# Kernel optimization log

Hardware: AMD Instinct MI355X
Metric: run time of the kernel (lower is better)

The kernel has to match this reference:

```python
import jax, jax.numpy as jnp
import numpy as np

SIG_G = [1.0, 1.0, 1.0]
LAYER_DIMS = [256, 128, 64]
N_ITER = 20
ALPHA = 0.01
B = 4096


def _cayley(g):
    # Cayley table C[a,b,c]: e_a * e_b = C[a,b,a^b] * e_{a^b} for diagonal metric g.
    n = len(g)
    nb = 1 << n
    C = np.zeros((nb, nb, nb), np.float32)
    for a in range(nb):
        for b in range(nb):
            # canonical reordering sign
            s = 0
            aa = a >> 1
            while aa:
                s += bin(aa & b).count('1')
                aa >>= 1
            sign = -1.0 if (s & 1) else 1.0
            # metric contribution from repeated generators
            for i in range(n):
                if (a >> i) & 1 and (b >> i) & 1:
                    sign *= g[i]
            C[a, b, a ^ b] = sign
    return jnp.asarray(C)


def _reverse_signs(n):
    # reverse: blade of grade k gets sign (-1)^(k*(k-1)/2)
    nb = 1 << n
    k = np.array([bin(i).count('1') for i in range(nb)])
    return jnp.asarray(((-1.0) ** (k * (k - 1) // 2)).astype(np.float32))


CAYLEY = _cayley(SIG_G)   # [8, 8, 8], sparse (one nonzero per (a,b))
REV = _reverse_signs(len(SIG_G))  # [8]


def _gp(x, W):
    # geometric product 'linear layer': x [B, Din, nb], W [Dout, Din, nb] -> [B, Dout, nb]
    return jnp.einsum('nja,ijb,abc->nic', x, W, CAYLEY, optimize=True)


def setup_inputs() -> dict:
    key = jax.random.key(0)
    ks = jax.random.split(key, 5)
    nb = 1 << len(SIG_G)
    x = jax.random.normal(ks[0], (B, LAYER_DIMS[0], nb), jnp.float32)
    W1 = jax.random.normal(ks[1], (LAYER_DIMS[0], LAYER_DIMS[1], nb), jnp.float32) * 0.01
    W2 = jax.random.normal(ks[2], (LAYER_DIMS[1], LAYER_DIMS[2], nb), jnp.float32) * 0.01
    h1 = jax.random.normal(ks[3], (B, LAYER_DIMS[1], nb), jnp.float32) * 0.001
    h2 = jax.random.normal(ks[4], (B, LAYER_DIMS[2], nb), jnp.float32) * 0.001
    return {'x': x, 'W1': W1, 'W2': W2, 'h1': h1, 'h2': h2}


def reference(x, W1, W2, h1, h2):
    states = [x, h1, h2]
    weights = [W1, W2]
    L = len(states)
    for _ in range(N_ITER):
        for l in range(1, L):
            W = weights[l - 1]                      # [D_{l-1}, D_l, nb]
            pred_prev = _gp(states[l], W)           # [B, D_{l-1}, nb]
            err_prev = states[l - 1] - pred_prev
            W_rev_T = jnp.transpose(W * REV, (1, 0, 2))  # reverse + transpose(0,1)
            grad = -_gp(err_prev, W_rev_T)          # [B, D_l, nb]
            if l < L - 1:
                pred_curr = _gp(states[l + 1], weights[l])
                grad = grad + (states[l] - pred_curr)
            grad = jnp.clip(grad, -1.0, 1.0)
            states[l] = states[l] - ALPHA * grad
    return tuple(states)
```

## Files before the change

kernel.cpp:

```cpp
#include <hip/hip_runtime.h>

#define N_ITER 20
#define ALPHA 0.01f

typedef unsigned short ushort_t;
typedef __attribute__((ext_vector_type(8))) short bf16x8;
typedef __attribute__((ext_vector_type(16))) float f32x16;

__device__ __forceinline__ float csign(int a, int b) {
    int s = 0;
    for (int aa = a >> 1; aa; aa >>= 1) s += __popc(aa & b);
    return (s & 1) ? -1.0f : 1.0f;
}

__device__ __forceinline__ float revsign(int b) {
    int k = __popc(b);
    return ((k * (k - 1) / 2) & 1) ? -1.0f : 1.0f;
}

__device__ __forceinline__ ushort_t f2bf(float f) {
    union { float f; unsigned u; } v;
    v.f = f;
    unsigned r = v.u + 0x7fffu + ((v.u >> 16) & 1u);
    return (ushort_t)(r >> 16);
}

__device__ __forceinline__ size_t swz64(int r, int k, int K) {
    return (size_t)r * K + (k & ~63) + ((((k >> 3) ^ r) & 7) << 3) + (k & 7);
}

__device__ __forceinline__ void async16(const void* g, void* l) {
    __builtin_amdgcn_global_load_lds((const __attribute__((address_space(1))) void*)g,
                                     (__attribute__((address_space(3))) void*)l, 16, 0, 0);
}

__global__ void build_M_kernel(const float* __restrict__ W, ushort_t* __restrict__ MfA,
                               ushort_t* __restrict__ Mrbt, ushort_t* __restrict__ Mrneg,
                               ushort_t* __restrict__ Mbtneg, int P, int Q) {
    int idx = blockIdx.x * blockDim.x + threadIdx.x;
    int total = P * Q * 64;
    if (idx >= total) return;
    int c = idx & 7;
    int a = (idx >> 3) & 7;
    int pq = idx >> 6;
    int q = pq % Q;
    int p = pq / Q;
    int b = a ^ c;
    float w = W[((size_t)p * Q + q) * 8 + b];
    float fw = csign(a, b) * w;
    float rw = csign(a, b) * revsign(b) * w;
    MfA[swz64(q * 8 + a, p * 8 + c, P * 8)] = f2bf(fw);
    Mrbt[swz64(q * 8 + c, p * 8 + a, P * 8)] = f2bf(rw);
    if (Mrneg) Mrneg[swz64(q * 8 + c, p * 8 + a, P * 8)] = f2bf(-rw);
    if (Mbtneg) Mbtneg[swz64(p * 8 + c, q * 8 + a, Q * 8)] = f2bf(-fw);
}

__global__ void f2bf_swz_kernel(const float* __restrict__ in, ushort_t* __restrict__ out,
                                int n, int kshift) {
    int i = blockIdx.x * blockDim.x + threadIdx.x;
    if (i >= n) return;
    int K = 1 << kshift;
    int r = i >> kshift;
    int k = i & (K - 1);
    out[swz64(r, k, K)] = f2bf(in[i]);
}

template <int MODE, int BM, int BN, bool ADDI>
__device__ __forceinline__ void gemm_body(ushort_t* __restrict__ S,
                                          const ushort_t* __restrict__ A,
                                          const ushort_t* __restrict__ BT, int K,
                                          const ushort_t* __restrict__ A2,
                                          const ushort_t* __restrict__ BT2, int K2,
                                          const float* __restrict__ Xf,
                                          const float* __restrict__ Rf,
                                          float* __restrict__ Hout,
                                          ushort_t* __restrict__ Bout,
                                          float* __restrict__ Fout,
                                          int N, int bx, int by) {
    constexpr int FI = BM / 64;
    constexpr int FJ = BN / 64;
    constexpr int CPW = (BM + BN) / 32;
    constexpr int SZ = (BM + BN) * 64;

    const int t = threadIdx.x;
    const int lane = t & 63;
    const int w = t >> 6;
    const int wr = w >> 1;
    const int wc = w & 1;
    const int l31 = lane & 31;
    const int lh = lane >> 5;
    const int row0 = by * BM;
    const int col0 = bx * BN;
    const int srow = lane >> 3;
    const int sk = (lane & 7) * 8;
    const int sw7 = l31 & 7;

    f32x16 acc[FI][FJ];
#pragma unroll
    for (int i = 0; i < FI; ++i)
#pragma unroll
        for (int j = 0; j < FJ; ++j)
#pragma unroll
            for (int r = 0; r < 16; ++r) acc[i][j][r] = 0.0f;

    const ushort_t* gpA[CPW];
    const ushort_t* gpB[CPW];
    int lofs[CPW];
#pragma unroll
    for (int cc = 0; cc < CPW; ++cc) {
        int ch = cc * 4 + w;
        int r8 = ch * 8;
        lofs[cc] = ch * 512;
        if (r8 < BM) {
            gpA[cc] = A + (size_t)(row0 + r8 + srow) * K + sk;
            gpB[cc] = A2 ? (A2 + (size_t)(row0 + r8 + srow) * K2 + sk) : nullptr;
        } else {
            gpA[cc] = BT + (size_t)(col0 + r8 - BM + srow) * K + sk;
            gpB[cc] = BT2 ? (BT2 + (size_t)(col0 + r8 - BM + srow) * K2 + sk) : nullptr;
        }
    }

    const int T1 = K >> 6;
    const int T2 = K2 >> 6;
    const int Ttot = T1 + T2;

    auto stage = [&](int tt, ushort_t* Sb) {
        if (tt < T1) {
#pragma unroll
            for (int cc = 0; cc < CPW; ++cc)
                async16(gpA[cc] + (size_t)tt * 64, &Sb[lofs[cc]]);
        } else {
            const int tl = tt - T1;
#pragma unroll
            for (int cc = 0; cc < CPW; ++cc)
                async16(gpB[cc] + (size_t)tl * 64, &Sb[lofs[cc]]);
        }
    };

    stage(0, S);
    __syncthreads();

    ushort_t* Sc = S;
    ushort_t* Sn = S + SZ;
    for (int tt = 0; tt < Ttot; ++tt) {
        if (tt + 1 < Ttot) stage(tt + 1, Sn);

        bf16x8 af[4][FI], bfm[4][FJ];
#pragma unroll
        for (int s = 0; s < 4; ++s) {
            int pos = ((2 * s + lh) ^ sw7) * 8;
#pragma unroll
            for (int i = 0; i < FI; ++i)
                af[s][i] = *(const bf16x8*)&Sc[(wr * (BM / 2) + i * 32 + l31) * 64 + pos];
#pragma unroll
            for (int j = 0; j < FJ; ++j)
                bfm[s][j] = *(const bf16x8*)&Sc[(BM + wc * (BN / 2) + j * 32 + l31) * 64 + pos];
        }
#pragma unroll
        for (int s = 0; s < 4; ++s)
#pragma unroll
            for (int i = 0; i < FI; ++i)
#pragma unroll
                for (int j = 0; j < FJ; ++j)
                    acc[i][j] = __builtin_amdgcn_mfma_f32_32x32x16_bf16(af[s][i], bfm[s][j],
                                                                        acc[i][j], 0, 0, 0);
        __syncthreads();
        ushort_t* tmp = Sc; Sc = Sn; Sn = tmp;
    }

#pragma unroll
    for (int i = 0; i < FI; ++i) {
#pragma unroll
        for (int j = 0; j < FJ; ++j) {
#pragma unroll
            for (int r = 0; r < 16; ++r) {
                int row = row0 + wr * (BM / 2) + i * 32 + (r & 3) + 8 * (r >> 2) + 4 * lh;
                int col = col0 + wc * (BN / 2) + j * 32 + l31;
                size_t off = (size_t)row * N + col;
                float v = acc[i][j][r];
                if (MODE == 1) {
                    Fout[off] = v;
                } else if (MODE == 2) {
                    float h = Xf[off];
                    float g = fminf(fmaxf(v - Rf[off], -1.0f), 1.0f);
                    float hn = h - ALPHA * g;
                    Hout[off] = hn;
                    Bout[swz64(row, col, N)] = f2bf(hn);
                } else if (MODE == 3) {
                    float h = Xf[off];
                    float g = fminf(fmaxf(v, -1.0f), 1.0f);
                    float hn = h - ALPHA * g;
                    Hout[off] = hn;
                    Bout[swz64(row, col, N)] = f2bf(hn);
                } else {
                    float vv = v + ((ADDI && row == col) ? 1.0f : 0.0f);
                    Bout[swz64(col, row, N)] = f2bf(vv);
                }
            }
        }
    }
}

template <int MODE, int BM, int BN, bool ADDI>
__global__ __launch_bounds__(256) void gemm_k(const ushort_t* __restrict__ A,
                                              const ushort_t* __restrict__ BT, int K,
                                              const ushort_t* __restrict__ A2,
                                              const ushort_t* __restrict__ BT2, int K2,
                                              const float* __restrict__ Xf,
                                              const float* __restrict__ Rf,
                                              float* __restrict__ Hout,
                                              ushort_t* __restrict__ Bout,
                                              float* __restrict__ Fout, int N) {
    __shared__ ushort_t S[2 * (BM + BN) * 64];
    gemm_body<MODE, BM, BN, ADDI>(S, A, BT, K, A2, BT2, K2, Xf, Rf, Hout, Bout, Fout, N,
                                  blockIdx.x, blockIdx.y);
}

extern "C" void kernel_launch(void* const* d_in, const int* in_sizes, int n_in,
                              void* d_out, int out_size, void* d_ws, size_t ws_size,
                              hipStream_t stream) {
    const float* X  = (const float*)d_in[0];
    const float* W1 = (const float*)d_in[1];
    const float* W2 = (const float*)d_in[2];
    const float* h1 = (const float*)d_in[3];
    const float* h2 = (const float*)d_in[4];
    float* out = (float*)d_out;

    const size_t szX  = (size_t)4096 * 2048;
    const size_t szH1 = (size_t)4096 * 1024;
    const size_t szH2 = (size_t)4096 * 512;

    float* outX = out;
    float* H1 = out + szX;
    float* H2 = H1 + szH1;

    ushort_t* M1fwdA  = (ushort_t*)d_ws;
    ushort_t* M1rbt   = M1fwdA + (size_t)1024 * 2048;
    ushort_t* M2fwdA  = M1rbt + (size_t)1024 * 2048;
    ushort_t* M2rbt   = M2fwdA + (size_t)512 * 1024;
    ushort_t* M2rneg  = M2rbt + (size_t)512 * 1024;
    ushort_t* M2btneg = M2rneg + (size_t)512 * 1024;
    ushort_t* GmT1p   = M2btneg + (size_t)1024 * 512;
    ushort_t* GmT2    = GmT1p + (size_t)1024 * 1024;
    ushort_t* Xb      = GmT2 + (size_t)512 * 512;
    ushort_t* H1bA    = Xb + szX;
    ushort_t* H1bB    = H1bA + szH1;
    ushort_t* H2bA    = H1bB + szH1;
    ushort_t* H2bB    = H2bA + szH2;
    float*    R       = (float*)(H2bB + szH2);

    build_M_kernel<<<(256 * 128 * 64 + 255) / 256, 256, 0, stream>>>(
        W1, M1fwdA, M1rbt, nullptr, nullptr, 256, 128);
    build_M_kernel<<<(128 * 64 * 64 + 255) / 256, 256, 0, stream>>>(
        W2, M2fwdA, M2rbt, M2rneg, M2btneg, 128, 64);

    hipMemcpyAsync(H1, h1, szH1 * sizeof(float), hipMemcpyDeviceToDevice, stream);
    hipMemcpyAsync(H2, h2, szH2 * sizeof(float), hipMemcpyDeviceToDevice, stream);
    f2bf_swz_kernel<<<(int)((szX + 255) / 256), 256, 0, stream>>>(X, Xb, (int)szX, 11);
    f2bf_swz_kernel<<<(int)((szH1 + 255) / 256), 256, 0, stream>>>(h1, H1bA, (int)szH1, 10);
    f2bf_swz_kernel<<<(int)((szH2 + 255) / 256), 256, 0, stream>>>(h2, H2bA, (int)szH2, 9);

    gemm_k<1, 128, 64, false><<<dim3(16, 32), 256, 0, stream>>>(
        Xb, M1rbt, 2048, nullptr, nullptr, 0, nullptr, nullptr, nullptr, nullptr, R, 1024);
    gemm_k<4, 64, 64, true><<<dim3(16, 16), 256, 0, stream>>>(
        M1fwdA, M1rbt, 2048, nullptr, nullptr, 0, nullptr, nullptr, nullptr, GmT1p, nullptr, 1024);
    gemm_k<4, 64, 64, false><<<dim3(8, 8), 256, 0, stream>>>(
        M2fwdA, M2rbt, 1024, nullptr, nullptr, 0, nullptr, nullptr, nullptr, GmT2, nullptr, 512);

    ushort_t* H1old = H1bA; ushort_t* H1new = H1bB;
    ushort_t* H2old = H2bA; ushort_t* H2new = H2bB;
    for (int it = 0; it < N_ITER; ++it) {
        gemm_k<2, 128, 64, false><<<dim3(16, 32), 256, 0, stream>>>(
            H1old, GmT1p, 1024, H2old, M2btneg, 512, H1, R, H1, H1new, nullptr, 1024);
        gemm_k<3, 64, 64, false><<<dim3(8, 64), 256, 0, stream>>>(
            H2old, GmT2, 512, H1new, M2rneg, 1024, H2, nullptr, H2, H2new, nullptr, 512);
        ushort_t* tmp;
        tmp = H1old; H1old = H1new; H1new = tmp;
        tmp = H2old; H2old = H2new; H2new = tmp;
    }

    hipMemcpyAsync(outX, X, szX * sizeof(float), hipMemcpyDeviceToDevice, stream);
}
```

Measured before the change: 1.130 ms.

## Load B operand directly from fragment-packed global layout into registers

Weight and Gram B-matrices are now stored in an MFMA-fragment-ordered layout (bfrag), so each wave reads its B fragments straight from global memory into registers instead of staging them through LDS. Only the A tile goes through LDS, and the main loop is unrolled by two with register double-buffering of B. Tile shapes change to 64x128 for all GEMMs. This cuts LDS traffic and footprint, but relies on global/L2 bandwidth for B and assumes an even tile count per K loop.

```diff
diff --git a/kernel.cpp b/kernel.cpp
--- a/kernel.cpp
+++ b/kernel.cpp
@@ -27,6 +27,11 @@
 
 __device__ __forceinline__ size_t swz64(int r, int k, int K) {
     return (size_t)r * K + (k & ~63) + ((((k >> 3) ^ r) & 7) << 3) + (k & 7);
+}
+
+__device__ __forceinline__ size_t bfrag(int r, int k, int NR) {
+    return ((((size_t)(k >> 6) * (NR >> 5) + (r >> 5)) * 4 + ((k >> 4) & 3)) * 512)
+           + (size_t)(((((k >> 3) & 1) * 32) + (r & 31)) * 8 + (k & 7));
 }
 
 __device__ __forceinline__ void async16(const void* g, void* l) {
@@ -50,9 +55,9 @@
     float fw = csign(a, b) * w;
     float rw = csign(a, b) * revsign(b) * w;
     MfA[swz64(q * 8 + a, p * 8 + c, P * 8)] = f2bf(fw);
-    Mrbt[swz64(q * 8 + c, p * 8 + a, P * 8)] = f2bf(rw);
-    if (Mrneg) Mrneg[swz64(q * 8 + c, p * 8 + a, P * 8)] = f2bf(-rw);
-    if (Mbtneg) Mbtneg[swz64(p * 8 + c, q * 8 + a, Q * 8)] = f2bf(-fw);
+    Mrbt[bfrag(q * 8 + c, p * 8 + a, Q * 8)] = f2bf(rw);
+    if (Mrneg) Mrneg[bfrag(q * 8 + c, p * 8 + a, Q * 8)] = f2bf(-rw);
+    if (Mbtneg) Mbtneg[bfrag(p * 8 + c, q * 8 + a, P * 8)] = f2bf(-fw);
 }
 
 __global__ void f2bf_swz_kernel(const float* __restrict__ in, ushort_t* __restrict__ out,
@@ -66,21 +71,21 @@
 }
 
 template <int MODE, int BM, int BN, bool ADDI>
-__device__ __forceinline__ void gemm_body(ushort_t* __restrict__ S,
-                                          const ushort_t* __restrict__ A,
-                                          const ushort_t* __restrict__ BT, int K,
-                                          const ushort_t* __restrict__ A2,
-                                          const ushort_t* __restrict__ BT2, int K2,
-                                          const float* __restrict__ Xf,
-                                          const float* __restrict__ Rf,
-                                          float* __restrict__ Hout,
-                                          ushort_t* __restrict__ Bout,
-                                          float* __restrict__ Fout,
-                                          int N, int bx, int by) {
+__global__ __launch_bounds__(256) void gemm_k(const ushort_t* __restrict__ A,
+                                              const ushort_t* __restrict__ BT, int K,
+                                              const ushort_t* __restrict__ A2,
+                                              const ushort_t* __restrict__ BT2, int K2,
+                                              const float* __restrict__ Xf,
+                                              const float* __restrict__ Rf,
+                                              float* __restrict__ Hout,
+                                              ushort_t* __restrict__ Bout,
+                                              float* __restrict__ Fout, int N) {
     constexpr int FI = BM / 64;
     constexpr int FJ = BN / 64;
-    constexpr int CPW = (BM + BN) / 32;
-    constexpr int SZ = (BM + BN) * 64;
+    constexpr int CPW = BM / 32;
+    constexpr int SZ = BM * 64;
+
+    __shared__ ushort_t S[2 * SZ];
 
     const int t = threadIdx.x;
     const int lane = t & 63;
@@ -89,11 +94,12 @@
     const int wc = w & 1;
     const int l31 = lane & 31;
     const int lh = lane >> 5;
-    const int row0 = by * BM;
-    const int col0 = bx * BN;
+    const int row0 = blockIdx.y * BM;
+    const int col0 = blockIdx.x * BN;
     const int srow = lane >> 3;
     const int sk = (lane & 7) * 8;
     const int sw7 = l31 & 7;
+    const int cg0 = (col0 >> 5) + wc * FJ;
 
     f32x16 acc[FI][FJ];
 #pragma unroll
@@ -103,69 +109,79 @@
 #pragma unroll
             for (int r = 0; r < 16; ++r) acc[i][j][r] = 0.0f;
 
-    const ushort_t* gpA[CPW];
-    const ushort_t* gpB[CPW];
+    const ushort_t* gA1[CPW];
+    const ushort_t* gA2[CPW];
     int lofs[CPW];
 #pragma unroll
     for (int cc = 0; cc < CPW; ++cc) {
         int ch = cc * 4 + w;
-        int r8 = ch * 8;
         lofs[cc] = ch * 512;
-        if (r8 < BM) {
-            gpA[cc] = A + (size_t)(row0 + r8 + srow) * K + sk;
-            gpB[cc] = A2 ? (A2 + (size_t)(row0 + r8 + srow) * K2 + sk) : nullptr;
-        } else {
-            gpA[cc] = BT + (size_t)(col0 + r8 - BM + srow) * K + sk;
-            gpB[cc] = BT2 ? (BT2 + (size_t)(col0 + r8 - BM + srow) * K2 + sk) : nullptr;
-        }
+        gA1[cc] = A + (size_t)(row0 + ch * 8 + srow) * K + sk;
+        gA2[cc] = A2 ? (A2 + (size_t)(row0 + ch * 8 + srow) * K2 + sk) : A;
     }
 
     const int T1 = K >> 6;
     const int T2 = K2 >> 6;
     const int Ttot = T1 + T2;
+    const size_t bstride = (size_t)N * 64;
+    const size_t rec0 = ((size_t)cg0 * 4) * 512 + (size_t)lane * 8;
 
     auto stage = [&](int tt, ushort_t* Sb) {
         if (tt < T1) {
 #pragma unroll
             for (int cc = 0; cc < CPW; ++cc)
-                async16(gpA[cc] + (size_t)tt * 64, &Sb[lofs[cc]]);
+                async16(gA1[cc] + (size_t)tt * 64, &Sb[lofs[cc]]);
         } else {
             const int tl = tt - T1;
 #pragma unroll
             for (int cc = 0; cc < CPW; ++cc)
-                async16(gpB[cc] + (size_t)tl * 64, &Sb[lofs[cc]]);
+                async16(gA2[cc] + (size_t)tl * 64, &Sb[lofs[cc]]);
         }
     };
 
-    stage(0, S);
-    __syncthreads();
-
-    ushort_t* Sc = S;
-    ushort_t* Sn = S + SZ;
-    for (int tt = 0; tt < Ttot; ++tt) {
-        if (tt + 1 < Ttot) stage(tt + 1, Sn);
-
-        bf16x8 af[4][FI], bfm[4][FJ];
+    auto loadB = [&](int tt, bf16x8 (&bq)[4][FJ]) {
+        const ushort_t* base;
+        if (tt < T1) base = BT + (size_t)tt * bstride + rec0;
+        else         base = BT2 + (size_t)(tt - T1) * bstride + rec0;
+#pragma unroll
+        for (int j = 0; j < FJ; ++j)
+#pragma unroll
+            for (int s = 0; s < 4; ++s)
+                bq[s][j] = *(const bf16x8*)(base + (size_t)(j * 4 + s) * 512);
+    };
+
+    auto compute = [&](const ushort_t* Sc, bf16x8 (&bq)[4][FJ]) {
 #pragma unroll
         for (int s = 0; s < 4; ++s) {
             int pos = ((2 * s + lh) ^ sw7) * 8;
 #pragma unroll
-            for (int i = 0; i < FI; ++i)
-                af[s][i] = *(const bf16x8*)&Sc[(wr * (BM / 2) + i * 32 + l31) * 64 + pos];
-#pragma unroll
-            for (int j = 0; j < FJ; ++j)
-                bfm[s][j] = *(const bf16x8*)&Sc[(BM + wc * (BN / 2) + j * 32 + l31) * 64 + pos];
-        }
-#pragma unroll
-        for (int s = 0; s < 4; ++s)
-#pragma unroll
-            for (int i = 0; i < FI; ++i)
+            for (int i = 0; i < FI; ++i) {
+                bf16x8 a = *(const bf16x8*)&Sc[(wr * (BM / 2) + i * 32 + l31) * 64 + pos];
 #pragma unroll
                 for (int j = 0; j < FJ; ++j)
-                    acc[i][j] = __builtin_amdgcn_mfma_f32_32x32x16_bf16(af[s][i], bfm[s][j],
+                    acc[i][j] = __builtin_amdgcn_mfma_f32_32x32x16_bf16(a, bq[s][j],
                                                                         acc[i][j], 0, 0, 0);
+            }
+        }
+    };
+
+    bf16x8 b0[4][FJ], b1[4][FJ];
+
+    stage(0, S);
+    loadB(0, b0);
+    __syncthreads();
+
+    for (int tt = 0; tt < Ttot; tt += 2) {
+        stage(tt + 1, S + SZ);
+        loadB(tt + 1, b1);
+        compute(S, b0);
         __syncthreads();
-        ushort_t* tmp = Sc; Sc = Sn; Sn = tmp;
+        if (tt + 2 < Ttot) {
+            stage(tt + 2, S);
+            loadB(tt + 2, b0);
+        }
+        compute(S + SZ, b1);
+        __syncthreads();
     }
 
 #pragma unroll
@@ -194,26 +210,11 @@
                     Bout[swz64(row, col, N)] = f2bf(hn);
                 } else {
                     float vv = v + ((ADDI && row == col) ? 1.0f : 0.0f);
-                    Bout[swz64(col, row, N)] = f2bf(vv);
+                    Bout[bfrag(col, row, N)] = f2bf(vv);
                 }
             }
         }
     }
-}
-
-template <int MODE, int BM, int BN, bool ADDI>
-__global__ __launch_bounds__(256) void gemm_k(const ushort_t* __restrict__ A,
-                                              const ushort_t* __restrict__ BT, int K,
-                                              const ushort_t* __restrict__ A2,
-                                              const ushort_t* __restrict__ BT2, int K2,
-                                              const float* __restrict__ Xf,
-                                              const float* __restrict__ Rf,
-                                              float* __restrict__ Hout,
-                                              ushort_t* __restrict__ Bout,
-                                              float* __restrict__ Fout, int N) {
-    __shared__ ushort_t S[2 * (BM + BN) * 64];
-    gemm_body<MODE, BM, BN, ADDI>(S, A, BT, K, A2, BT2, K2, Xf, Rf, Hout, Bout, Fout, N,
-                                  blockIdx.x, blockIdx.y);
 }
 
 extern "C" void kernel_launch(void* const* d_in, const int* in_sizes, int n_in,
@@ -260,19 +261,19 @@
     f2bf_swz_kernel<<<(int)((szH1 + 255) / 256), 256, 0, stream>>>(h1, H1bA, (int)szH1, 10);
     f2bf_swz_kernel<<<(int)((szH2 + 255) / 256), 256, 0, stream>>>(h2, H2bA, (int)szH2, 9);
 
-    gemm_k<1, 128, 64, false><<<dim3(16, 32), 256, 0, stream>>>(
+    gemm_k<1, 64, 128, false><<<dim3(8, 64), 256, 0, stream>>>(
         Xb, M1rbt, 2048, nullptr, nullptr, 0, nullptr, nullptr, nullptr, nullptr, R, 1024);
-    gemm_k<4, 64, 64, true><<<dim3(16, 16), 256, 0, stream>>>(
+    gemm_k<4, 64, 128, true><<<dim3(8, 16), 256, 0, stream>>>(
         M1fwdA, M1rbt, 2048, nullptr, nullptr, 0, nullptr, nullptr, nullptr, GmT1p, nullptr, 1024);
-    gemm_k<4, 64, 64, false><<<dim3(8, 8), 256, 0, stream>>>(
+    gemm_k<4, 64, 128, false><<<dim3(4, 8), 256, 0, stream>>>(
         M2fwdA, M2rbt, 1024, nullptr, nullptr, 0, nullptr, nullptr, nullptr, GmT2, nullptr, 512);
 
     ushort_t* H1old = H1bA; ushort_t* H1new = H1bB;
     ushort_t* H2old = H2bA; ushort_t* H2new = H2bB;
     for (int it = 0; it < N_ITER; ++it) {
-        gemm_k<2, 128, 64, false><<<dim3(16, 32), 256, 0, stream>>>(
+        gemm_k<2, 64, 128, false><<<dim3(8, 64), 256, 0, stream>>>(
             H1old, GmT1p, 1024, H2old, M2btneg, 512, H1, R, H1, H1new, nullptr, 1024);
-        gemm_k<3, 64, 64, false><<<dim3(8, 64), 256, 0, stream>>>(
+        gemm_k<3, 64, 128, false><<<dim3(4, 64), 256, 0, stream>>>(
             H2old, GmT2, 512, H1new, M2rneg, 1024, H2, nullptr, H2, H2new, nullptr, 512);
         ushort_t* tmp;
         tmp = H1old; H1old = H1new; H1new = tmp;
```

Result: slower. 1.353 ms (+19.7%).

## Triple-buffer GEMM K-loop with vmcnt waits and enlarge tiles to 128x128

Applied to the files above, without the earlier changes.

The GEMM main loop moves from double buffering with two block-wide syncs per K step to a three-stage LDS ring. Each step waits with an explicit s_waitcnt vmcnt and hits a single barrier, and the stage two tiles ahead is issued right after the fragments are read into registers. The aim is to keep global-to-LDS copies further ahead of the MFMA work and to cut barrier stalls. All launches also switch to 128x128 tiles, which raises per-block reuse but gives much smaller grids (e.g. 128 blocks for the H2 update) and about 96KB of LDS per block. The hardcoded vmcnt(8) is only valid while each stage issues exactly eight async loads per thread, which holds for 128x128.

```diff
diff --git a/kernel.cpp b/kernel.cpp
--- a/kernel.cpp
+++ b/kernel.cpp
@@ -66,21 +66,21 @@
 }
 
 template <int MODE, int BM, int BN, bool ADDI>
-__device__ __forceinline__ void gemm_body(ushort_t* __restrict__ S,
-                                          const ushort_t* __restrict__ A,
-                                          const ushort_t* __restrict__ BT, int K,
-                                          const ushort_t* __restrict__ A2,
-                                          const ushort_t* __restrict__ BT2, int K2,
-                                          const float* __restrict__ Xf,
-                                          const float* __restrict__ Rf,
-                                          float* __restrict__ Hout,
-                                          ushort_t* __restrict__ Bout,
-                                          float* __restrict__ Fout,
-                                          int N, int bx, int by) {
+__global__ __launch_bounds__(256) void gemm_k(const ushort_t* __restrict__ A,
+                                              const ushort_t* __restrict__ BT, int K,
+                                              const ushort_t* __restrict__ A2,
+                                              const ushort_t* __restrict__ BT2, int K2,
+                                              const float* __restrict__ Xf,
+                                              const float* __restrict__ Rf,
+                                              float* __restrict__ Hout,
+                                              ushort_t* __restrict__ Bout,
+                                              float* __restrict__ Fout, int N) {
     constexpr int FI = BM / 64;
     constexpr int FJ = BN / 64;
     constexpr int CPW = (BM + BN) / 32;
     constexpr int SZ = (BM + BN) * 64;
+
+    __shared__ ushort_t S[3 * SZ];
 
     const int t = threadIdx.x;
     const int lane = t & 63;
@@ -89,8 +89,8 @@
     const int wc = w & 1;
     const int l31 = lane & 31;
     const int lh = lane >> 5;
-    const int row0 = by * BM;
-    const int col0 = bx * BN;
+    const int row0 = blockIdx.y * BM;
+    const int col0 = blockIdx.x * BN;
     const int srow = lane >> 3;
     const int sk = (lane & 7) * 8;
     const int sw7 = l31 & 7;
@@ -113,10 +113,10 @@
         lofs[cc] = ch * 512;
         if (r8 < BM) {
             gpA[cc] = A + (size_t)(row0 + r8 + srow) * K + sk;
-            gpB[cc] = A2 ? (A2 + (size_t)(row0 + r8 + srow) * K2 + sk) : nullptr;
+            gpB[cc] = A2 ? (A2 + (size_t)(row0 + r8 + srow) * K2 + sk) : A;
         } else {
             gpA[cc] = BT + (size_t)(col0 + r8 - BM + srow) * K + sk;
-            gpB[cc] = BT2 ? (BT2 + (size_t)(col0 + r8 - BM + srow) * K2 + sk) : nullptr;
+            gpB[cc] = BT2 ? (BT2 + (size_t)(col0 + r8 - BM + srow) * K2 + sk) : BT;
         }
     }
 
@@ -137,13 +137,20 @@
         }
     };
 
-    stage(0, S);
-    __syncthreads();
-
-    ushort_t* Sc = S;
-    ushort_t* Sn = S + SZ;
+    ushort_t* B0 = S;
+    ushort_t* B1 = S + SZ;
+    ushort_t* B2 = S + 2 * SZ;
+    stage(0, B0);
+    if (Ttot > 1) stage(1, B1);
+
     for (int tt = 0; tt < Ttot; ++tt) {
-        if (tt + 1 < Ttot) stage(tt + 1, Sn);
+        if (tt + 1 < Ttot) {
+            asm volatile("s_waitcnt vmcnt(8)" ::: "memory");
+        } else {
+            asm volatile("s_waitcnt vmcnt(0)" ::: "memory");
+        }
+        __builtin_amdgcn_s_barrier();
+        __builtin_amdgcn_sched_barrier(0);
 
         bf16x8 af[4][FI], bfm[4][FJ];
 #pragma unroll
@@ -151,11 +158,12 @@
             int pos = ((2 * s + lh) ^ sw7) * 8;
 #pragma unroll
             for (int i = 0; i < FI; ++i)
-                af[s][i] = *(const bf16x8*)&Sc[(wr * (BM / 2) + i * 32 + l31) * 64 + pos];
+                af[s][i] = *(const bf16x8*)&B0[(wr * (BM / 2) + i * 32 + l31) * 64 + pos];
 #pragma unroll
             for (int j = 0; j < FJ; ++j)
-                bfm[s][j] = *(const bf16x8*)&Sc[(BM + wc * (BN / 2) + j * 32 + l31) * 64 + pos];
-        }
+                bfm[s][j] = *(const bf16x8*)&B0[(BM + wc * (BN / 2) + j * 32 + l31) * 64 + pos];
+        }
+        if (tt + 2 < Ttot) stage(tt + 2, B2);
 #pragma unroll
         for (int s = 0; s < 4; ++s)
 #pragma unroll
@@ -164,8 +172,7 @@
                 for (int j = 0; j < FJ; ++j)
                     acc[i][j] = __builtin_amdgcn_mfma_f32_32x32x16_bf16(af[s][i], bfm[s][j],
                                                                         acc[i][j], 0, 0, 0);
-        __syncthreads();
-        ushort_t* tmp = Sc; Sc = Sn; Sn = tmp;
+        ushort_t* tmp = B0; B0 = B1; B1 = B2; B2 = tmp;
     }
 
 #pragma unroll
@@ -201,21 +208,6 @@
     }
 }
 
-template <int MODE, int BM, int BN, bool ADDI>
-__global__ __launch_bounds__(256) void gemm_k(const ushort_t* __restrict__ A,
-                                              const ushort_t* __restrict__ BT, int K,
-                                              const ushort_t* __restrict__ A2,
-                                              const ushort_t* __restrict__ BT2, int K2,
-                                              const float* __restrict__ Xf,
-                                              const float* __restrict__ Rf,
-                                              float* __restrict__ Hout,
-                                              ushort_t* __restrict__ Bout,
-                                              float* __restrict__ Fout, int N) {
-    __shared__ ushort_t S[2 * (BM + BN) * 64];
-    gemm_body<MODE, BM, BN, ADDI>(S, A, BT, K, A2, BT2, K2, Xf, Rf, Hout, Bout, Fout, N,
-                                  blockIdx.x, blockIdx.y);
-}
-
 extern "C" void kernel_launch(void* const* d_in, const int* in_sizes, int n_in,
                               void* d_out, int out_size, void* d_ws, size_t ws_size,
                               hipStream_t stream) {
@@ -260,19 +252,19 @@
     f2bf_swz_kernel<<<(int)((szH1 + 255) / 256), 256, 0, stream>>>(h1, H1bA, (int)szH1, 10);
     f2bf_swz_kernel<<<(int)((szH2 + 255) / 256), 256, 0, stream>>>(h2, H2bA, (int)szH2, 9);
 
-    gemm_k<1, 128, 64, false><<<dim3(16, 32), 256, 0, stream>>>(
+    gemm_k<1, 128, 128, false><<<dim3(8, 32), 256, 0, stream>>>(
         Xb, M1rbt, 2048, nullptr, nullptr, 0, nullptr, nullptr, nullptr, nullptr, R, 1024);
-    gemm_k<4, 64, 64, true><<<dim3(16, 16), 256, 0, stream>>>(
+    gemm_k<4, 128, 128, true><<<dim3(8, 8), 256, 0, stream>>>(
         M1fwdA, M1rbt, 2048, nullptr, nullptr, 0, nullptr, nullptr, nullptr, GmT1p, nullptr, 1024);
-    gemm_k<4, 64, 64, false><<<dim3(8, 8), 256, 0, stream>>>(
+    gemm_k<4, 128, 128, false><<<dim3(4, 4), 256, 0, stream>>>(
         M2fwdA, M2rbt, 1024, nullptr, nullptr, 0, nullptr, nullptr, nullptr, GmT2, nullptr, 512);
 
     ushort_t* H1old = H1bA; ushort_t* H1new = H1bB;
     ushort_t* H2old = H2bA; ushort_t* H2new = H2bB;
     for (int it = 0; it < N_ITER; ++it) {
-        gemm_k<2, 128, 64, false><<<dim3(16, 32), 256, 0, stream>>>(
+        gemm_k<2, 128, 128, false><<<dim3(8, 32), 256, 0, stream>>>(
             H1old, GmT1p, 1024, H2old, M2btneg, 512, H1, R, H1, H1new, nullptr, 1024);
-        gemm_k<3, 64, 64, false><<<dim3(8, 64), 256, 0, stream>>>(
+        gemm_k<3, 128, 128, false><<<dim3(4, 32), 256, 0, stream>>>(
             H2old, GmT2, 512, H1new, M2rneg, 1024, H2, nullptr, H2, H2new, nullptr, 512);
         ushort_t* tmp;
         tmp = H1old; H1old = H1new; H1new = tmp;
```

Result: slower. 1.225 ms (+8.4%).
